# Kernel tuning notes

Measured on AMD Instinct MI355X. Metric: run time of the kernel, lower is better.

Reference implementation:

```python
import jax, jax.numpy as jnp
from jax import lax
import numpy as np

NA, NC = 3, 1
CONF_THRESH, IOU_THRESH = 0.5, 0.5


def _conv(x, w, b, pad):
    y = lax.conv_general_dilated(x, w, (1, 1), [(pad, pad), (pad, pad)],
                                 dimension_numbers=('NCHW', 'OIHW', 'NCHW'))
    return y + b[None, :, None, None]


def _maxpool2(x):
    return lax.reduce_window(x, -jnp.inf, lax.max, (1, 1, 2, 2), (1, 1, 2, 2), 'VALID')


def _stream(x, w1, b1, w2, b2):
    x = _maxpool2(jax.nn.relu(_conv(x, w1, b1, 1)))
    x = _maxpool2(jax.nn.relu(_conv(x, w2, b2, 1)))
    return x


def _pairwise_iou(b):
    # b: [N,4] in (x1,y1,x2,y2); matches torchvision box_iou (no area clamp)
    x1, y1, x2, y2 = b[:, 0], b[:, 1], b[:, 2], b[:, 3]
    area = (x2 - x1) * (y2 - y1)
    ix1 = jnp.maximum(x1[:, None], x1[None, :])
    iy1 = jnp.maximum(y1[:, None], y1[None, :])
    ix2 = jnp.minimum(x2[:, None], x2[None, :])
    iy2 = jnp.minimum(y2[:, None], y2[None, :])
    inter = jnp.clip(ix2 - ix1, 0.0) * jnp.clip(iy2 - iy1, 0.0)
    return inter / (area[:, None] + area[None, :] - inter)


def _nms_keep(boxes, scores, conf_keep, iou_thresh):
    # Greedy NMS over a fixed, small N; returns bool keep mask (conf + NMS).
    n = boxes.shape[0]
    order = jnp.argsort(-jnp.where(conf_keep, scores, -jnp.inf))
    iou = _pairwise_iou(boxes[order])  # [N,N] in score order
    idx = jnp.arange(n)

    def body(i, state):
        keep, suppressed = state
        valid = jnp.logical_not(suppressed[i])
        keep = keep.at[i].set(valid)
        suppressed = suppressed | (valid & (iou[i] > iou_thresh) & (idx > i))
        return keep, suppressed

    keep_sorted, _ = lax.fori_loop(0, n, body,
                                   (jnp.zeros(n, bool), jnp.zeros(n, bool)))
    keep = jnp.zeros(n, bool).at[order].set(keep_sorted)
    return keep & conf_keep


def setup_inputs() -> dict:
    key = jax.random.key(0)
    ks = jax.random.split(key, 14)
    s = 0.05
    inp = {
        'x': jax.random.normal(ks[0], (8, 3, 512, 512), jnp.float32),
        'rgb_w1': jax.random.normal(ks[1], (32, 3, 3, 3), jnp.float32) * s,
        'rgb_b1': jnp.zeros((32,), jnp.float32),
        'rgb_w2': jax.random.normal(ks[2], (64, 32, 3, 3), jnp.float32) * s,
        'rgb_b2': jnp.zeros((64,), jnp.float32),
        'ir_w1': jax.random.normal(ks[3], (32, 3, 3, 3), jnp.float32) * s,
        'ir_b1': jnp.zeros((32,), jnp.float32),
        'ir_w2': jax.random.normal(ks[4], (64, 32, 3, 3), jnp.float32) * s,
        'ir_b2': jnp.zeros((64,), jnp.float32),
        'fuse_w': jax.random.normal(ks[5], (128, 128, 3, 3), jnp.float32) * s,
        'fuse_b': jnp.zeros((128,), jnp.float32),
        'det_w': jax.random.normal(ks[6], (NA * (5 + NC), 128, 1, 1), jnp.float32),
        'det_b': jax.random.normal(ks[7], (NA * (5 + NC),), jnp.float32),
    }
    return inp


def reference(x, rgb_w1, rgb_b1, rgb_w2, rgb_b2,
              ir_w1, ir_b1, ir_w2, ir_b2,
              fuse_w, fuse_b, det_w, det_b):
    f1 = _stream(x, rgb_w1, rgb_b1, rgb_w2, rgb_b2)   # [B,64,H/4,W/4]
    f2 = _stream(x, ir_w1, ir_b1, ir_w2, ir_b2)       # [B,64,H/4,W/4]
    f = jnp.concatenate([f1, f2], axis=1)             # [B,128,H/4,W/4]
    f = jax.nn.relu(_conv(f, fuse_w, fuse_b, 1))
    f = jnp.mean(f, axis=(2, 3), keepdims=True)       # AdaptiveAvgPool2d((1,1))
    p = _conv(f, det_w, det_b, 0)                     # [B,18,1,1]
    B, C, H, W = p.shape
    p = p.reshape(B, NA, 5 + NC, H, W).transpose(0, 1, 3, 4, 2)  # [B,na,H,W,5+nc]
    boxes = p[..., :4].reshape(B, -1, 4)              # [B, na*H*W, 4]
    scores = jax.nn.sigmoid(p[..., 4]).reshape(B, -1) # [B, na*H*W]
    conf_keep = scores > CONF_THRESH
    keep = jax.vmap(_nms_keep, in_axes=(0, 0, 0, None))(boxes, scores, conf_keep,
                                                        IOU_THRESH)
    # Fixed-shape equivalent of the per-image variable-length preds list:
    # preds[b] == boxes[b][keep[b]].
    return p, boxes, scores, keep
```

## Files before the change

### kernel.cpp

```cpp
#include <hip/hip_runtime.h>
#include <math.h>


typedef __bf16 bf16x8 __attribute__((ext_vector_type(8)));
typedef float f32x4 __attribute__((ext_vector_type(4)));

static __device__ __forceinline__ ushort f2bf(float f) {
    unsigned u = __float_as_uint(f);
    unsigned r = (u + 0x7fffu + ((u >> 16) & 1u)) >> 16;
    return (ushort)r;
}
static __device__ __forceinline__ float bf2f(ushort h) {
    return __uint_as_float(((unsigned)h) << 16);
}

__global__ __launch_bounds__(256) void w1prep(
    const float* __restrict__ w_rgb, const float* __restrict__ w_ir,
    uint* __restrict__ W1p)
{
    int i = blockIdx.x * 256 + threadIdx.x;
    if (i >= 2048) return;
    int s = i >> 10, r = i & 1023;
    int oc = r >> 5, k = r & 31;
    const float* w = s ? w_ir : w_rgb;
    float v = (k < 27) ? w[oc * 27 + k] : 0.f;
    ushort h = f2bf(v);
    W1p[i] = (uint)h | ((uint)f2bf(v - bf2f(h)) << 16);
}

__global__ __launch_bounds__(256) void conv1_mfma(
    const float* __restrict__ x, const uint* __restrict__ W1p,
    const float* __restrict__ bias, ushort* __restrict__ C1h,
    ushort* __restrict__ C1l)
{
    __shared__ uint S[3 * 4 * 132];
    __shared__ float pool[4][32][32];

    const int seg = blockIdx.x, Y = blockIdx.y, b = blockIdx.z;
    const int tid = threadIdx.x, wsub = tid >> 6, lane = tid & 63;
    const int n = lane & 15, q = lane >> 4;

    uint4 bu0a = *(const uint4*)&W1p[n * 32 + q * 8];
    uint4 bu0b = *(const uint4*)&W1p[n * 32 + q * 8 + 4];
    uint4 bu1a = *(const uint4*)&W1p[(16 + n) * 32 + q * 8];
    uint4 bu1b = *(const uint4*)&W1p[(16 + n) * 32 + q * 8 + 4];

    const int ih0 = 2 * Y - 1, iw0 = seg * 128 - 1;
    for (int i = tid; i < 1584; i += 256) {
        int c = i / 528, rem = i - c * 528;
        int r = rem / 132, cc = rem - r * 132;
        int ih = ih0 + r, iw = iw0 + cc;
        float v = 0.f;
        if (cc < 130 && ih >= 0 && ih < 512 && iw >= 0 && iw < 512)
            v = x[((b * 3 + c) * 512 + ih) * 512 + iw];
        ushort h = f2bf(v);
        S[i] = (uint)h | ((uint)f2bf(v - bf2f(h)) << 16);
    }

    uint4 bh0v, bl0v, bh1v, bl1v;
    {
        uint u0[8], u1[8];
        *(uint4*)&u0[0] = bu0a; *(uint4*)&u0[4] = bu0b;
        *(uint4*)&u1[0] = bu1a; *(uint4*)&u1[4] = bu1b;
        uint* bh0 = (uint*)&bh0v; uint* bl0 = (uint*)&bl0v;
        uint* bh1 = (uint*)&bh1v; uint* bl1 = (uint*)&bl1v;
#pragma unroll
        for (int j = 0; j < 4; ++j) {
            bh0[j] = (u0[2 * j] & 0xffffu) | (u0[2 * j + 1] << 16);
            bl0[j] = (u0[2 * j] >> 16) | (u0[2 * j + 1] & 0xffff0000u);
            bh1[j] = (u1[2 * j] & 0xffffu) | (u1[2 * j + 1] << 16);
            bl1[j] = (u1[2 * j] >> 16) | (u1[2 * j + 1] & 0xffff0000u);
        }
    }
    bf16x8 Bh0 = __builtin_bit_cast(bf16x8, bh0v);
    bf16x8 Bl0 = __builtin_bit_cast(bf16x8, bl0v);
    bf16x8 Bh1 = __builtin_bit_cast(bf16x8, bh1v);
    bf16x8 Bl1 = __builtin_bit_cast(bf16x8, bl1v);

    int idx[8];
    const int off0 = (wsub & 1) * 132 + (wsub >> 1) * 64 + n;
#pragma unroll
    for (int e = 0; e < 8; ++e) {
        int k = q * 8 + e;
        int c = (k >= 18) ? ((k >= 27) ? 3 : 2) : ((k >= 9) ? 1 : 0);
        int t = k - c * 9;
        int ky = (t >= 6) ? 2 : ((t >= 3) ? 1 : 0);
        int kx = t - ky * 3;
        idx[e] = (k < 27) ? ((c * 4 + ky) * 132 + kx + off0) : 0;
    }
    __syncthreads();

    f32x4 acc[4][2];
#pragma unroll
    for (int mt = 0; mt < 4; ++mt)
#pragma unroll
        for (int nt = 0; nt < 2; ++nt) acc[mt][nt] = (f32x4){0.f, 0.f, 0.f, 0.f};

#pragma unroll
    for (int mt = 0; mt < 4; ++mt) {
        uint u[8];
#pragma unroll
        for (int e = 0; e < 8; ++e) u[e] = S[idx[e] + mt * 16];
        uint4 ahv, alv;
        uint* ah = (uint*)&ahv;
        uint* al = (uint*)&alv;
#pragma unroll
        for (int j = 0; j < 4; ++j) {
            ah[j] = (u[2 * j] & 0xffffu) | (u[2 * j + 1] << 16);
            al[j] = (u[2 * j] >> 16) | (u[2 * j + 1] & 0xffff0000u);
        }
        bf16x8 Ah = __builtin_bit_cast(bf16x8, ahv);
        bf16x8 Al = __builtin_bit_cast(bf16x8, alv);
        acc[mt][0] = __builtin_amdgcn_mfma_f32_16x16x32_bf16(Ah, Bh0, acc[mt][0], 0, 0, 0);
        acc[mt][1] = __builtin_amdgcn_mfma_f32_16x16x32_bf16(Ah, Bh1, acc[mt][1], 0, 0, 0);
        acc[mt][0] = __builtin_amdgcn_mfma_f32_16x16x32_bf16(Ah, Bl0, acc[mt][0], 0, 0, 0);
        acc[mt][1] = __builtin_amdgcn_mfma_f32_16x16x32_bf16(Ah, Bl1, acc[mt][1], 0, 0, 0);
        acc[mt][0] = __builtin_amdgcn_mfma_f32_16x16x32_bf16(Al, Bh0, acc[mt][0], 0, 0, 0);
        acc[mt][1] = __builtin_amdgcn_mfma_f32_16x16x32_bf16(Al, Bh1, acc[mt][1], 0, 0, 0);
    }

#pragma unroll
    for (int mt = 0; mt < 4; ++mt)
#pragma unroll
        for (int nt = 0; nt < 2; ++nt) {
            int oc = nt * 16 + n;
            int plx = mt * 8 + q * 2;
            pool[wsub][plx][oc]     = fmaxf(acc[mt][nt][0], acc[mt][nt][1]);
            pool[wsub][plx + 1][oc] = fmaxf(acc[mt][nt][2], acc[mt][nt][3]);
        }
    __syncthreads();
    {
        int plx = tid >> 2, ocq = tid & 3;
        int wp = plx >> 5, pl = plx & 31;
        __attribute__((aligned(16))) ushort hb[8], lb[8];
#pragma unroll
        for (int e = 0; e < 8; ++e) {
            int oc = ocq * 8 + e;
            float v = fmaxf(pool[wp * 2][pl][oc], pool[wp * 2 + 1][pl][oc]);
            v = fmaxf(v + bias[oc], 0.f);
            ushort h = f2bf(v);
            hb[e] = h;
            lb[e] = f2bf(v - bf2f(h));
        }
        int ow = seg * 64 + plx;
        size_t base = (((size_t)((b * 256 + Y) * 256 + ow)) << 5) + ocq * 8;
        *(uint4*)(C1h + base) = *(const uint4*)hb;
        *(uint4*)(C1l + base) = *(const uint4*)lb;
    }
}

__global__ __launch_bounds__(256) void conv2_mfma(
    const ushort* __restrict__ C1h, const ushort* __restrict__ C1l,
    const float* __restrict__ w2, const float* __restrict__ bias,
    ushort* __restrict__ Ahi, ushort* __restrict__ Alo, int stream_base)
{
    __shared__ char lds[40960];
    ushort* Bh = (ushort*)lds;
    ushort* Bl = (ushort*)(lds + 20480);
    float (*pool)[32][64] = (float (*)[32][64])lds;

    const int seg = blockIdx.x, Y = blockIdx.y, b = blockIdx.z;
    const int tid = threadIdx.x, wsub = tid >> 6, lane = tid & 63;
    const int n = lane & 15, q = lane >> 4;
    const int yc = 2 * Y + (wsub & 1);
    const int wx0 = seg * 128 + (wsub >> 1) * 64;

    const uint4 zero4 = make_uint4(0u, 0u, 0u, 0u);

    auto stageB = [&](int t0, int ntap) {
        for (int i = tid; i < ntap * 2048; i += 256) {
            int t = t0 + (i >> 11), r = i & 2047;
            float v = w2[r * 9 + t];
            ushort h = f2bf(v);
            Bh[i] = h;
            Bl[i] = f2bf(v - bf2f(h));
        }
    };

    auto loadA = [&](int t, uint4* aH, uint4* aL) {
        int ky = t / 3, kx = t - ky * 3;
        int yy = yc + ky - 1;
        bool yok = (yy >= 0) & (yy < 256);
#pragma unroll
        for (int mt = 0; mt < 4; ++mt) {
            int xp = wx0 + mt * 16 + n + kx - 1;
            bool ok = yok & (xp >= 0) & (xp < 256);
            int yyc = ok ? yy : 0, xpc = ok ? xp : 0;
            size_t off = (((size_t)((b * 256 + yyc) * 256 + xpc)) << 5) + q * 8;
            aH[mt] = ok ? *(const uint4*)(C1h + off) : zero4;
            aL[mt] = ok ? *(const uint4*)(C1l + off) : zero4;
        }
    };

    f32x4 acc[4][4];
#pragma unroll
    for (int mt = 0; mt < 4; ++mt)
#pragma unroll
        for (int nt = 0; nt < 4; ++nt) acc[mt][nt] = (f32x4){0.f, 0.f, 0.f, 0.f};

    uint4 aH[4], aL[4];
    loadA(0, aH, aL);
    stageB(0, 5);
    __syncthreads();

    for (int t = 0; t < 9; ++t) {
        if (t == 5) {
            __syncthreads();
            stageB(5, 4);
            __syncthreads();
        }
        const int rel = (t < 5) ? t : t - 5;
        uint4 cH[4], cL[4];
#pragma unroll
        for (int mt = 0; mt < 4; ++mt) { cH[mt] = aH[mt]; cL[mt] = aL[mt]; }
        if (t + 1 < 9) loadA(t + 1, aH, aL);
        bf16x8 bh[4], bl[4];
#pragma unroll
        for (int nt = 0; nt < 4; ++nt) {
            int off = rel * 2048 + (nt * 16 + n) * 32 + q * 8;
            bh[nt] = __builtin_bit_cast(bf16x8, *(const uint4*)&Bh[off]);
            bl[nt] = __builtin_bit_cast(bf16x8, *(const uint4*)&Bl[off]);
        }
#pragma unroll
        for (int mt = 0; mt < 4; ++mt) {
            bf16x8 ah = __builtin_bit_cast(bf16x8, cH[mt]);
#pragma unroll
            for (int nt = 0; nt < 4; ++nt)
                acc[mt][nt] = __builtin_amdgcn_mfma_f32_16x16x32_bf16(ah, bh[nt], acc[mt][nt], 0, 0, 0);
        }
#pragma unroll
        for (int mt = 0; mt < 4; ++mt) {
            bf16x8 ah = __builtin_bit_cast(bf16x8, cH[mt]);
#pragma unroll
            for (int nt = 0; nt < 4; ++nt)
                acc[mt][nt] = __builtin_amdgcn_mfma_f32_16x16x32_bf16(ah, bl[nt], acc[mt][nt], 0, 0, 0);
        }
#pragma unroll
        for (int mt = 0; mt < 4; ++mt) {
            bf16x8 al = __builtin_bit_cast(bf16x8, cL[mt]);
#pragma unroll
            for (int nt = 0; nt < 4; ++nt)
                acc[mt][nt] = __builtin_amdgcn_mfma_f32_16x16x32_bf16(al, bh[nt], acc[mt][nt], 0, 0, 0);
        }
    }

    __syncthreads();

#pragma unroll
    for (int mt = 0; mt < 4; ++mt)
#pragma unroll
        for (int nt = 0; nt < 4; ++nt) {
            int oc = nt * 16 + n;
            int plx = mt * 8 + q * 2;
            pool[wsub][plx][oc]     = fmaxf(acc[mt][nt][0], acc[mt][nt][1]);
            pool[wsub][plx + 1][oc] = fmaxf(acc[mt][nt][2], acc[mt][nt][3]);
        }
    __syncthreads();

    {
        int plx = tid >> 2, ocq = tid & 3;
        int wp = plx >> 5, pl = plx & 31;
        __attribute__((aligned(16))) ushort hb[16], lb[16];
#pragma unroll
        for (int e = 0; e < 16; ++e) {
            int oc = ocq * 16 + e;
            float v = fmaxf(pool[wp * 2][pl][oc], pool[wp * 2 + 1][pl][oc]);
            v = fmaxf(v + bias[oc], 0.f);
            ushort h = f2bf(v);
            hb[e] = h;
            lb[e] = f2bf(v - bf2f(h));
        }
        int gx = seg * 64 + plx;
        int cpl = (stream_base >> 5) + (ocq >> 1);
        int cho = (ocq & 1) * 16;
        size_t base = (((size_t)(((b * 4 + cpl) * 128 + Y) * 128 + gx)) << 5) + cho;
        uint4* dh = (uint4*)(Ahi + base);
        uint4* dl = (uint4*)(Alo + base);
        dh[0] = *(const uint4*)&hb[0];
        dh[1] = *(const uint4*)&hb[8];
        dl[0] = *(const uint4*)&lb[0];
        dl[1] = *(const uint4*)&lb[8];
    }
}

__global__ __launch_bounds__(256) void wprep(
    const float* __restrict__ fw, ushort* __restrict__ Whi,
    ushort* __restrict__ Wlo)
{
    int idx = blockIdx.x * 256 + threadIdx.x;
    if (idx >= 147456) return;
    int kk = idx & 31;
    int oc = (idx >> 5) & 127;
    int ct = idx >> 12;
    int c = ct / 9, t = ct - c * 9;
    int ic = c * 32 + kk;
    int ky = t / 3, kx = t - ky * 3;
    float v = fw[((oc * 128 + ic) * 3 + ky) * 3 + kx];
    ushort h = f2bf(v);
    Whi[idx] = h;
    Wlo[idx] = f2bf(v - bf2f(h));
}

__global__ __launch_bounds__(256, 2) void fuse_mfma(
    const ushort* __restrict__ Ahi, const ushort* __restrict__ Alo,
    const ushort* __restrict__ Whi, const ushort* __restrict__ Wlo,
    const float* __restrict__ bias, float* __restrict__ featsum)
{
    __shared__ float partial[4][128];
    const int b = blockIdx.x, ypair = blockIdx.y;
    const int tid = threadIdx.x, wsub = tid >> 6, lane = tid & 63;
    const int n = lane & 15, q = lane >> 4;
    const int y = ypair * 2 + (wsub >> 1);
    const int xbase = (wsub & 1) * 64;

    f32x4 acc[4][8];
#pragma unroll
    for (int mt = 0; mt < 4; ++mt)
#pragma unroll
        for (int g = 0; g < 8; ++g) acc[mt][g] = (f32x4){0.f, 0.f, 0.f, 0.f};

    const uint4 zero4 = make_uint4(0u, 0u, 0u, 0u);

    auto loadA = [&](int tc, uint4* oh, uint4* ol) {
        int c = tc / 9, t = tc - c * 9;
        int ky = t / 3, kx = t - ky * 3;
        int yy = y + ky - 1;
        bool yok = (yy >= 0) & (yy < 128);
#pragma unroll
        for (int mt = 0; mt < 4; ++mt) {
            int xp = xbase + mt * 16 + n + kx - 1;
            bool ok = yok & (xp >= 0) & (xp < 128);
            int yyc = ok ? yy : 0, xpc = ok ? xp : 0;
            size_t aoff = (((size_t)(((b * 4 + c) * 128 + yyc) * 128 + xpc)) << 5) + q * 8;
            oh[mt] = ok ? *(const uint4*)(Ahi + aoff) : zero4;
            ol[mt] = ok ? *(const uint4*)(Alo + aoff) : zero4;
        }
    };

    uint4 pAh[4], pAl[4];
    loadA(0, pAh, pAl);

    const ushort* WhiB = Whi + n * 32 + q * 8;
    const ushort* WloB = Wlo + n * 32 + q * 8;

    uint4 nBh[4], nBl[4];
#pragma unroll
    for (int j = 0; j < 4; ++j) {
        nBh[j] = *(const uint4*)(WhiB + j * 512);
        nBl[j] = *(const uint4*)(WloB + j * 512);
    }

    for (int tc = 0; tc < 36; ++tc) {
        uint4 cAh[4], cAl[4];
#pragma unroll
        for (int mt = 0; mt < 4; ++mt) { cAh[mt] = pAh[mt]; cAl[mt] = pAl[mt]; }
        if (tc + 1 < 36) loadA(tc + 1, pAh, pAl);
#pragma unroll
        for (int g = 0; g < 8; ++g) {
            const int slot = g & 3;
            bf16x8 bh = __builtin_bit_cast(bf16x8, nBh[slot]);
            bf16x8 bl = __builtin_bit_cast(bf16x8, nBl[slot]);
            {
                size_t off = (size_t)(tc * 8 + g + 4) * 512;
                nBh[slot] = *(const uint4*)(WhiB + off);
                nBl[slot] = *(const uint4*)(WloB + off);
            }
#pragma unroll
            for (int mt = 0; mt < 4; ++mt) {
                bf16x8 ah = __builtin_bit_cast(bf16x8, cAh[mt]);
                acc[mt][g] = __builtin_amdgcn_mfma_f32_16x16x32_bf16(ah, bh, acc[mt][g], 0, 0, 0);
            }
#pragma unroll
            for (int mt = 0; mt < 4; ++mt) {
                bf16x8 ah = __builtin_bit_cast(bf16x8, cAh[mt]);
                acc[mt][g] = __builtin_amdgcn_mfma_f32_16x16x32_bf16(ah, bl, acc[mt][g], 0, 0, 0);
            }
#pragma unroll
            for (int mt = 0; mt < 4; ++mt) {
                bf16x8 al = __builtin_bit_cast(bf16x8, cAl[mt]);
                acc[mt][g] = __builtin_amdgcn_mfma_f32_16x16x32_bf16(al, bh, acc[mt][g], 0, 0, 0);
            }
        }
    }

#pragma unroll
    for (int g = 0; g < 8; ++g) {
        float bv = bias[g * 16 + n];
        float v = 0.f;
#pragma unroll
        for (int mt = 0; mt < 4; ++mt)
#pragma unroll
            for (int r = 0; r < 4; ++r) v += fmaxf(acc[mt][g][r] + bv, 0.f);
        v += __shfl_xor(v, 16);
        v += __shfl_xor(v, 32);
        if (lane < 16) partial[wsub][g * 16 + lane] = v;
    }
    __syncthreads();
    if (tid < 128) {
        float v = partial[0][tid] + partial[1][tid] + partial[2][tid] + partial[3][tid];
        atomicAdd(&featsum[b * 128 + tid], v);
    }
}

__global__ void det_nms(const float* __restrict__ featsum,
                        const float* __restrict__ dw, const float* __restrict__ db,
                        float* __restrict__ out)
{
    const int b = threadIdx.x;
    if (b >= 8) return;
    const float inv = 1.0f / 16384.0f;

    float p[18];
    for (int j = 0; j < 18; ++j) {
        float a = db[j];
        const float* wp = &dw[j * 128];
        const float* f = &featsum[b * 128];
        for (int c = 0; c < 128; ++c) a = fmaf(wp[c], f[c] * inv, a);
        p[j] = a;
    }
    for (int a = 0; a < 3; ++a)
        for (int e = 0; e < 6; ++e) out[b * 18 + a * 6 + e] = p[a * 6 + e];

    float bx[3][4], sc[3];
    bool ck[3];
    for (int a = 0; a < 3; ++a) {
        for (int k = 0; k < 4; ++k) {
            bx[a][k] = p[a * 6 + k];
            out[144 + b * 12 + a * 4 + k] = bx[a][k];
        }
        float sg = 1.f / (1.f + expf(-p[a * 6 + 4]));
        sc[a] = sg;
        ck[a] = sg > 0.5f;
        out[240 + b * 3 + a] = sg;
    }

    float key[3];
    int order[3];
    bool used[3] = {false, false, false};
    for (int a = 0; a < 3; ++a) key[a] = ck[a] ? sc[a] : -INFINITY;
    for (int i = 0; i < 3; ++i) {
        int best = -1;
        float bk = 0.f;
        for (int a = 0; a < 3; ++a) {
            if (used[a]) continue;
            if (best < 0 || key[a] > bk) { best = a; bk = key[a]; }
        }
        order[i] = best;
        used[best] = true;
    }

    float X1[3], Y1[3], X2[3], Y2[3], AR[3];
    for (int i = 0; i < 3; ++i) {
        int o = order[i];
        X1[i] = bx[o][0]; Y1[i] = bx[o][1];
        X2[i] = bx[o][2]; Y2[i] = bx[o][3];
        AR[i] = (X2[i] - X1[i]) * (Y2[i] - Y1[i]);
    }
    bool suppressed[3] = {false, false, false}, keep_s[3];
    for (int i = 0; i < 3; ++i) {
        bool valid = !suppressed[i];
        keep_s[i] = valid;
        if (valid) {
            for (int j = i + 1; j < 3; ++j) {
                float ix1 = fmaxf(X1[i], X1[j]), iy1 = fmaxf(Y1[i], Y1[j]);
                float ix2 = fminf(X2[i], X2[j]), iy2 = fminf(Y2[i], Y2[j]);
                float inter = fmaxf(ix2 - ix1, 0.f) * fmaxf(iy2 - iy1, 0.f);
                float iou = inter / (AR[i] + AR[j] - inter);
                if (iou > 0.5f) suppressed[j] = true;
            }
        }
    }
    bool keep[3];
    for (int i = 0; i < 3; ++i) keep[order[i]] = keep_s[i];
    for (int a = 0; a < 3; ++a)
        out[264 + b * 3 + a] = (keep[a] && ck[a]) ? 1.f : 0.f;
}

__global__ void zero_feat(float* __restrict__ p)
{
    int i = blockIdx.x * 256 + threadIdx.x;
    if (i < 1024) p[i] = 0.f;
}

extern "C" void kernel_launch(void* const* d_in, const int* in_sizes, int n_in,
                              void* d_out, int out_size, void* d_ws, size_t ws_size,
                              hipStream_t stream)
{
    const float* x      = (const float*)d_in[0];
    const float* rgb_w1 = (const float*)d_in[1];
    const float* rgb_b1 = (const float*)d_in[2];
    const float* rgb_w2 = (const float*)d_in[3];
    const float* rgb_b2 = (const float*)d_in[4];
    const float* ir_w1  = (const float*)d_in[5];
    const float* ir_b1  = (const float*)d_in[6];
    const float* ir_w2  = (const float*)d_in[7];
    const float* ir_b2  = (const float*)d_in[8];
    const float* fuse_w = (const float*)d_in[9];
    const float* fuse_b = (const float*)d_in[10];
    const float* det_w  = (const float*)d_in[11];
    const float* det_b  = (const float*)d_in[12];
    float* out = (float*)d_out;

    char* ws = (char*)d_ws;
    ushort* C1h  = (ushort*)(ws);
    ushort* C1l  = (ushort*)(ws + 33554432);
    ushort* Whi  = (ushort*)(ws);
    ushort* Wlo  = (ushort*)(ws + 299008);
    float*  feat = (float*)(ws + 598016);
    ushort* Ahi  = (ushort*)(ws + 67108864);
    ushort* Alo  = (ushort*)(ws + 100663296);
    uint*   W1p  = (uint*)(ws + 134209536);

    dim3 blk(256);
    hipLaunchKernelGGL(w1prep, dim3(8), blk, 0, stream, rgb_w1, ir_w1, W1p);
    hipLaunchKernelGGL(conv1_mfma, dim3(4, 256, 8), blk, 0, stream, x, W1p, rgb_b1, C1h, C1l);
    hipLaunchKernelGGL(conv2_mfma, dim3(2, 128, 8), blk, 0, stream, C1h, C1l, rgb_w2, rgb_b2, Ahi, Alo, 0);
    hipLaunchKernelGGL(conv1_mfma, dim3(4, 256, 8), blk, 0, stream, x, W1p + 1024, ir_b1, C1h, C1l);
    hipLaunchKernelGGL(conv2_mfma, dim3(2, 128, 8), blk, 0, stream, C1h, C1l, ir_w2, ir_b2, Ahi, Alo, 64);
    hipLaunchKernelGGL(wprep, dim3(576), blk, 0, stream, fuse_w, Whi, Wlo);
    hipLaunchKernelGGL(zero_feat, dim3(4), blk, 0, stream, feat);
    hipLaunchKernelGGL(fuse_mfma, dim3(8, 64), blk, 0, stream, Ahi, Alo, Whi, Wlo, fuse_b, feat);
    hipLaunchKernelGGL(det_nms, dim3(1), dim3(64), 0, stream, feat, det_w, det_b, out);
}
```

Measured before the change: 512.6 us.

## Shrink fuse conv tile to one row per block and double-buffer A loads

The fuse convolution kernel now gives each block a single output row, with each wave covering 32 pixels instead of 64. This halves the accumulator registers, raises the occupancy hint from 2 to 3 blocks per SIMD, and doubles the grid size. The A-operand loads become a two-deep ping-pong prefetch and the MFMA issue is interleaved across two output groups. In exchange, each B weight fragment is reused over fewer pixels, so weight traffic per MFMA doubles.

```diff
diff --git a/kernel.cpp b/kernel.cpp
--- a/kernel.cpp
+++ b/kernel.cpp
@@ -301,21 +301,20 @@
     Wlo[idx] = f2bf(v - bf2f(h));
 }
 
-__global__ __launch_bounds__(256, 2) void fuse_mfma(
+__global__ __launch_bounds__(256, 3) void fuse_mfma(
     const ushort* __restrict__ Ahi, const ushort* __restrict__ Alo,
     const ushort* __restrict__ Whi, const ushort* __restrict__ Wlo,
     const float* __restrict__ bias, float* __restrict__ featsum)
 {
     __shared__ float partial[4][128];
-    const int b = blockIdx.x, ypair = blockIdx.y;
+    const int b = blockIdx.x, y = blockIdx.y;
     const int tid = threadIdx.x, wsub = tid >> 6, lane = tid & 63;
     const int n = lane & 15, q = lane >> 4;
-    const int y = ypair * 2 + (wsub >> 1);
-    const int xbase = (wsub & 1) * 64;
-
-    f32x4 acc[4][8];
-#pragma unroll
-    for (int mt = 0; mt < 4; ++mt)
+    const int xbase = wsub * 32;
+
+    f32x4 acc[2][8];
+#pragma unroll
+    for (int mt = 0; mt < 2; ++mt)
 #pragma unroll
         for (int g = 0; g < 8; ++g) acc[mt][g] = (f32x4){0.f, 0.f, 0.f, 0.f};
 
@@ -327,7 +326,7 @@
         int yy = y + ky - 1;
         bool yok = (yy >= 0) & (yy < 128);
 #pragma unroll
-        for (int mt = 0; mt < 4; ++mt) {
+        for (int mt = 0; mt < 2; ++mt) {
             int xp = xbase + mt * 16 + n + kx - 1;
             bool ok = yok & (xp >= 0) & (xp < 128);
             int yyc = ok ? yy : 0, xpc = ok ? xp : 0;
@@ -337,9 +336,6 @@
         }
     };
 
-    uint4 pAh[4], pAl[4];
-    loadA(0, pAh, pAl);
-
     const ushort* WhiB = Whi + n * 32 + q * 8;
     const ushort* WloB = Wlo + n * 32 + q * 8;
 
@@ -350,37 +346,50 @@
         nBl[j] = *(const uint4*)(WloB + j * 512);
     }
 
-    for (int tc = 0; tc < 36; ++tc) {
-        uint4 cAh[4], cAl[4];
-#pragma unroll
-        for (int mt = 0; mt < 4; ++mt) { cAh[mt] = pAh[mt]; cAl[mt] = pAl[mt]; }
-        if (tc + 1 < 36) loadA(tc + 1, pAh, pAl);
-#pragma unroll
-        for (int g = 0; g < 8; ++g) {
-            const int slot = g & 3;
-            bf16x8 bh = __builtin_bit_cast(bf16x8, nBh[slot]);
-            bf16x8 bl = __builtin_bit_cast(bf16x8, nBl[slot]);
+    uint4 A0h[2], A0l[2], A1h[2], A1l[2];
+    loadA(0, A0h, A0l);
+    loadA(1, A1h, A1l);
+
+    auto process = [&](uint4* bAh, uint4* bAl, int tc, bool pf) {
+        bf16x8 a0h = __builtin_bit_cast(bf16x8, bAh[0]);
+        bf16x8 a1h = __builtin_bit_cast(bf16x8, bAh[1]);
+        bf16x8 a0l = __builtin_bit_cast(bf16x8, bAl[0]);
+        bf16x8 a1l = __builtin_bit_cast(bf16x8, bAl[1]);
+#pragma unroll
+        for (int gp = 0; gp < 4; ++gp) {
+            const int g0 = 2 * gp, g1 = g0 + 1;
+            const int sl0 = g0 & 3, sl1 = g1 & 3;
+            bf16x8 bh0 = __builtin_bit_cast(bf16x8, nBh[sl0]);
+            bf16x8 bl0 = __builtin_bit_cast(bf16x8, nBl[sl0]);
+            bf16x8 bh1 = __builtin_bit_cast(bf16x8, nBh[sl1]);
+            bf16x8 bl1 = __builtin_bit_cast(bf16x8, nBl[sl1]);
             {
-                size_t off = (size_t)(tc * 8 + g + 4) * 512;
-                nBh[slot] = *(const uint4*)(WhiB + off);
-                nBl[slot] = *(const uint4*)(WloB + off);
+                size_t o0 = (size_t)(tc * 8 + g0 + 4) * 512;
+                size_t o1 = (size_t)(tc * 8 + g1 + 4) * 512;
+                nBh[sl0] = *(const uint4*)(WhiB + o0);
+                nBl[sl0] = *(const uint4*)(WloB + o0);
+                nBh[sl1] = *(const uint4*)(WhiB + o1);
+                nBl[sl1] = *(const uint4*)(WloB + o1);
             }
-#pragma unroll
-            for (int mt = 0; mt < 4; ++mt) {
-                bf16x8 ah = __builtin_bit_cast(bf16x8, cAh[mt]);
-                acc[mt][g] = __builtin_amdgcn_mfma_f32_16x16x32_bf16(ah, bh, acc[mt][g], 0, 0, 0);
-            }
-#pragma unroll
-            for (int mt = 0; mt < 4; ++mt) {
-                bf16x8 ah = __builtin_bit_cast(bf16x8, cAh[mt]);
-                acc[mt][g] = __builtin_amdgcn_mfma_f32_16x16x32_bf16(ah, bl, acc[mt][g], 0, 0, 0);
-            }
-#pragma unroll
-            for (int mt = 0; mt < 4; ++mt) {
-                bf16x8 al = __builtin_bit_cast(bf16x8, cAl[mt]);
-                acc[mt][g] = __builtin_amdgcn_mfma_f32_16x16x32_bf16(al, bh, acc[mt][g], 0, 0, 0);
-            }
-        }
+            acc[0][g0] = __builtin_amdgcn_mfma_f32_16x16x32_bf16(a0h, bh0, acc[0][g0], 0, 0, 0);
+            acc[1][g0] = __builtin_amdgcn_mfma_f32_16x16x32_bf16(a1h, bh0, acc[1][g0], 0, 0, 0);
+            acc[0][g1] = __builtin_amdgcn_mfma_f32_16x16x32_bf16(a0h, bh1, acc[0][g1], 0, 0, 0);
+            acc[1][g1] = __builtin_amdgcn_mfma_f32_16x16x32_bf16(a1h, bh1, acc[1][g1], 0, 0, 0);
+            acc[0][g0] = __builtin_amdgcn_mfma_f32_16x16x32_bf16(a0h, bl0, acc[0][g0], 0, 0, 0);
+            acc[1][g0] = __builtin_amdgcn_mfma_f32_16x16x32_bf16(a1h, bl0, acc[1][g0], 0, 0, 0);
+            acc[0][g1] = __builtin_amdgcn_mfma_f32_16x16x32_bf16(a0h, bl1, acc[0][g1], 0, 0, 0);
+            acc[1][g1] = __builtin_amdgcn_mfma_f32_16x16x32_bf16(a1h, bl1, acc[1][g1], 0, 0, 0);
+            acc[0][g0] = __builtin_amdgcn_mfma_f32_16x16x32_bf16(a0l, bh0, acc[0][g0], 0, 0, 0);
+            acc[1][g0] = __builtin_amdgcn_mfma_f32_16x16x32_bf16(a1l, bh0, acc[1][g0], 0, 0, 0);
+            acc[0][g1] = __builtin_amdgcn_mfma_f32_16x16x32_bf16(a0l, bh1, acc[0][g1], 0, 0, 0);
+            acc[1][g1] = __builtin_amdgcn_mfma_f32_16x16x32_bf16(a1l, bh1, acc[1][g1], 0, 0, 0);
+        }
+        if (pf) loadA(tc + 2, bAh, bAl);
+    };
+
+    for (int tcb = 0; tcb < 36; tcb += 2) {
+        process(A0h, A0l, tcb, tcb + 2 < 36);
+        process(A1h, A1l, tcb + 1, tcb + 3 < 36);
     }
 
 #pragma unroll
@@ -388,7 +397,7 @@
         float bv = bias[g * 16 + n];
         float v = 0.f;
 #pragma unroll
-        for (int mt = 0; mt < 4; ++mt)
+        for (int mt = 0; mt < 2; ++mt)
 #pragma unroll
             for (int r = 0; r < 4; ++r) v += fmaxf(acc[mt][g][r] + bv, 0.f);
         v += __shfl_xor(v, 16);
@@ -519,6 +528,6 @@
     hipLaunchKernelGGL(conv2_mfma, dim3(2, 128, 8), blk, 0, stream, C1h, C1l, ir_w2, ir_b2, Ahi, Alo, 64);
     hipLaunchKernelGGL(wprep, dim3(576), blk, 0, stream, fuse_w, Whi, Wlo);
     hipLaunchKernelGGL(zero_feat, dim3(4), blk, 0, stream, feat);
-    hipLaunchKernelGGL(fuse_mfma, dim3(8, 64), blk, 0, stream, Ahi, Alo, Whi, Wlo, fuse_b, feat);
+    hipLaunchKernelGGL(fuse_mfma, dim3(8, 128), blk, 0, stream, Ahi, Alo, Whi, Wlo, fuse_b, feat);
     hipLaunchKernelGGL(det_nms, dim3(1), dim3(64), 0, stream, feat, det_w, det_b, out);
 }
```

Result: slower. 576.8 us (+12.5%).
